# Kernel tuning notes

Measured on AMD Instinct MI355X. Metric: run time of the kernel, lower is better.

## Reference

```python
import jax, jax.numpy as jnp
import numpy as np

B, P, S, H, R = 32, 512, 1024, 1024, 256


def setup_inputs() -> dict:
    key = jax.random.key(0)
    k1, k2, k3 = jax.random.split(key, 3)
    pairs = jax.random.randint(k1, (B, P, 2, 2), 0, S, dtype=jnp.int64 if jax.config.jax_enable_x64 else jnp.int32)
    hidden_states = jax.random.normal(k2, (B, S, H), dtype=jnp.float32)
    W = jax.random.normal(k3, (R, 3 * H), dtype=jnp.float32) * (1.0 / np.sqrt(3 * H))
    b = jnp.zeros((R,), dtype=jnp.float32)
    return {"pairs": pairs, "hidden_states": hidden_states, "W": W, "b": b}


def reference(pairs, hidden_states, W, b):
    # pairs: [B, P, 2, 2] -> [:, :, 0, :] = (h_start, h_end), [:, :, 1, :] = (t_start, t_end)
    def gather_tokens(idx):  # idx: [B, P] -> [B, P, H]
        return jnp.take_along_axis(hidden_states, idx[:, :, None], axis=1)

    head_embed = 0.5 * (gather_tokens(pairs[:, :, 0, 0]) + gather_tokens(pairs[:, :, 0, 1]))
    tail_embed = 0.5 * (gather_tokens(pairs[:, :, 1, 0]) + gather_tokens(pairs[:, :, 1, 1]))
    feats = jnp.concatenate([head_embed, tail_embed, head_embed * tail_embed], axis=-1)  # [B, P, 3H]
    logits = jnp.einsum('bpf,rf->bpr', feats, W) + b  # [B, P, R]
    return logits
```

## Files before the change

kernel.cpp:

```cpp
#include <hip/hip_runtime.h>

#define NB 32
#define NP 512
#define NS 1024
#define NH 1024
#define NR 256
#define K3 3072

#define BM 64

typedef short short8 __attribute__((ext_vector_type(8)));
typedef __bf16 bf16x8 __attribute__((ext_vector_type(8)));
typedef float f32x4 __attribute__((ext_vector_type(4)));

__device__ __forceinline__ unsigned short f2bf(float f) {
  unsigned u = __builtin_bit_cast(unsigned, f);
  u += 0x7fffu + ((u >> 16) & 1u);
  return (unsigned short)(u >> 16);
}

__device__ __forceinline__ f32x4 mfma_bf16(short8 a, short8 b, f32x4 c) {
  return __builtin_amdgcn_mfma_f32_16x16x32_bf16(
      __builtin_bit_cast(bf16x8, a), __builtin_bit_cast(bf16x8, b), c, 0, 0, 0);
}

__device__ __forceinline__ void wg_barrier() {
  asm volatile("s_waitcnt lgkmcnt(0)" ::: "memory");
  __builtin_amdgcn_s_barrier();
}

__global__ void wconv_kernel(const float* __restrict__ W,
                             unsigned short* __restrict__ WbF) {
  int i = blockIdx.x * blockDim.x + threadIdx.x;
  int lane = i & 63, n16 = (i >> 6) & 15, kc = i >> 10;
  int lr = lane & 15, lg = lane >> 4;
  const float* src = W + (size_t)(n16 * 16 + lr) * K3 + kc * 32 + lg * 8;
  float4 a = *(const float4*)src;
  float4 b = *(const float4*)(src + 4);
  short8 o;
  o[0] = (short)f2bf(a.x); o[1] = (short)f2bf(a.y);
  o[2] = (short)f2bf(a.z); o[3] = (short)f2bf(a.w);
  o[4] = (short)f2bf(b.x); o[5] = (short)f2bf(b.y);
  o[6] = (short)f2bf(b.z); o[7] = (short)f2bf(b.w);
  *(short8*)(WbF + (size_t)i * 8) = o;
}

__global__ __launch_bounds__(512, 2) void gemm_kernel(
    const int* __restrict__ pairs, const float* __restrict__ hs,
    const unsigned short* __restrict__ WbF, const float* __restrict__ bias,
    float* __restrict__ out) {
  __shared__ __align__(16) unsigned short sA[2][3][BM][64];

  const int tid = threadIdx.x;
  const int blk = blockIdx.x;
  const int x     = blk & 7;
  const int jb    = blk >> 3;
  const int batch = x * 4 + (jb >> 3);
  const int mtile = jb & 7;
  const int m0    = (batch * 8 + mtile) * BM;

  const int pairi = tid >> 3;
  const int q     = tid & 7;
  int4 pr = ((const int4*)pairs)[m0 + pairi];
  const float* hb = hs + (size_t)batch * NS * NH + 8 * q;
  const float* rp[4];
  rp[0] = hb + (size_t)pr.x * NH;
  rp[1] = hb + (size_t)pr.y * NH;
  rp[2] = hb + (size_t)pr.z * NH;
  rp[3] = hb + (size_t)pr.w * NH;

  const int lane = tid & 63;
  const int w    = tid >> 6;
  const int lr   = lane & 15;
  const int lg   = lane >> 4;

  const unsigned short* wbase = WbF + (size_t)(w * 2) * 512 + (size_t)lane * 8;

  f32x4 acc[4][2];
#pragma unroll
  for (int i = 0; i < 4; ++i)
#pragma unroll
    for (int j = 0; j < 2; ++j) acc[i][j] = (f32x4){0.f, 0.f, 0.f, 0.f};

  float4 ldA[8], ldB[8];
  short8 wcur[12], wnxt[12];

  auto load_w = [&](int s, short8* wd) {
#pragma unroll
    for (int part = 0; part < 3; ++part)
#pragma unroll
      for (int ks = 0; ks < 2; ++ks)
#pragma unroll
        for (int j = 0; j < 2; ++j)
          wd[part * 4 + ks * 2 + j] = *(const short8*)(
              wbase + (size_t)(part * 32 + s * 2 + ks) * 8192 + (size_t)j * 512);
  };

  auto load_gather = [&](int s, float4* ld) {
    const int o = s * 64;
#pragma unroll
    for (int r = 0; r < 4; ++r) {
      ld[2 * r]     = *(const float4*)(rp[r] + o);
      ld[2 * r + 1] = *(const float4*)(rp[r] + o + 4);
    }
  };

  auto store_stage = [&](int buf, const float4* ld) {
    short8 hv, tv, pv;
#pragma unroll
    for (int e = 0; e < 8; ++e) {
      const int hi = e >> 2, ei = e & 3;
      float h = 0.5f * (((const float*)&ld[0 + hi])[ei] + ((const float*)&ld[2 + hi])[ei]);
      float t = 0.5f * (((const float*)&ld[4 + hi])[ei] + ((const float*)&ld[6 + hi])[ei]);
      float p = h * t;
      hv[e] = (short)f2bf(h); tv[e] = (short)f2bf(t); pv[e] = (short)f2bf(p);
    }
    const int col = (q ^ (pairi & 7)) * 8;
    *(short8*)&sA[buf][0][pairi][col] = hv;
    *(short8*)&sA[buf][1][pairi][col] = tv;
    *(short8*)&sA[buf][2][pairi][col] = pv;
  };

  auto compute = [&](int buf, short8* wc) {
#pragma unroll
    for (int ks = 0; ks < 2; ++ks) {
      short8 ah[4], at4[4], ap[4];
      const int col = (((ks * 4 + lg) ^ (lr & 7)) * 8);
#pragma unroll
      for (int i = 0; i < 4; ++i) {
        ah[i]  = *(const short8*)&sA[buf][0][i * 16 + lr][col];
        at4[i] = *(const short8*)&sA[buf][1][i * 16 + lr][col];
        ap[i]  = *(const short8*)&sA[buf][2][i * 16 + lr][col];
      }
#pragma unroll
      for (int j = 0; j < 2; ++j)
#pragma unroll
        for (int i = 0; i < 4; ++i) {
          acc[i][j] = mfma_bf16(ah[i],  wc[0 + ks * 2 + j], acc[i][j]);
          acc[i][j] = mfma_bf16(at4[i], wc[4 + ks * 2 + j], acc[i][j]);
          acc[i][j] = mfma_bf16(ap[i],  wc[8 + ks * 2 + j], acc[i][j]);
        }
    }
  };

  load_w(0, wcur);
  load_gather(0, ldA);
  load_gather(1, ldB);
  store_stage(0, ldA);

  auto stage = [&](int s, short8* wc, short8* wn, float4* gin, float4* gout) {
    wg_barrier();
    if (s < 15) load_w(s + 1, wn);
    if (s < 14) load_gather(s + 2, gin);
    compute(s & 1, wc);
    if (s < 15) store_stage((s & 1) ^ 1, gout);
  };

#pragma unroll 1
  for (int sp = 0; sp < 8; ++sp) {
    stage(2 * sp,     wcur, wnxt, ldA, ldB);
    stage(2 * sp + 1, wnxt, wcur, ldB, ldA);
  }

#pragma unroll
  for (int j = 0; j < 2; ++j) {
    const int col  = w * 32 + j * 16 + lr;
    const float bv = bias[col];
#pragma unroll
    for (int i = 0; i < 4; ++i) {
      const size_t rbase = (size_t)(m0 + i * 16 + lg * 4) * NR + col;
#pragma unroll
      for (int r = 0; r < 4; ++r)
        out[rbase + (size_t)r * NR] = acc[i][j][r] + bv;
    }
  }
}

extern "C" void kernel_launch(void* const* d_in, const int* in_sizes, int n_in,
                              void* d_out, int out_size, void* d_ws, size_t ws_size,
                              hipStream_t stream) {
  const int*   pairs = (const int*)d_in[0];
  const float* hs    = (const float*)d_in[1];
  const float* W     = (const float*)d_in[2];
  const float* bias  = (const float*)d_in[3];
  float* out = (float*)d_out;
  unsigned short* WbF = (unsigned short*)d_ws;

  wconv_kernel<<<(96 * 16 * 64) / 256, 256, 0, stream>>>(W, WbF);
  gemm_kernel<<<(NB * NP) / BM, 512, 0, stream>>>(pairs, hs, WbF, bias, out);
}
```

Before: 230.2 us.

## Pre-convert hidden states to half precision and switch MFMA to fp16

Measured after the change: 244.4 us. 1.06x slower.

```diff
diff --git a/kernel.cpp b/kernel.cpp
--- a/kernel.cpp
+++ b/kernel.cpp
@@ -9,19 +9,11 @@
 
 #define BM 64
 
-typedef short short8 __attribute__((ext_vector_type(8)));
-typedef __bf16 bf16x8 __attribute__((ext_vector_type(8)));
+typedef _Float16 half8 __attribute__((ext_vector_type(8)));
 typedef float f32x4 __attribute__((ext_vector_type(4)));
 
-__device__ __forceinline__ unsigned short f2bf(float f) {
-  unsigned u = __builtin_bit_cast(unsigned, f);
-  u += 0x7fffu + ((u >> 16) & 1u);
-  return (unsigned short)(u >> 16);
-}
-
-__device__ __forceinline__ f32x4 mfma_bf16(short8 a, short8 b, f32x4 c) {
-  return __builtin_amdgcn_mfma_f32_16x16x32_bf16(
-      __builtin_bit_cast(bf16x8, a), __builtin_bit_cast(bf16x8, b), c, 0, 0, 0);
+__device__ __forceinline__ f32x4 mfma_f16(half8 a, half8 b, f32x4 c) {
+  return __builtin_amdgcn_mfma_f32_16x16x32_f16(a, b, c, 0, 0, 0);
 }
 
 __device__ __forceinline__ void wg_barrier() {
@@ -30,26 +22,39 @@
 }
 
 __global__ void wconv_kernel(const float* __restrict__ W,
-                             unsigned short* __restrict__ WbF) {
+                             _Float16* __restrict__ WbF) {
   int i = blockIdx.x * blockDim.x + threadIdx.x;
   int lane = i & 63, n16 = (i >> 6) & 15, kc = i >> 10;
   int lr = lane & 15, lg = lane >> 4;
   const float* src = W + (size_t)(n16 * 16 + lr) * K3 + kc * 32 + lg * 8;
   float4 a = *(const float4*)src;
   float4 b = *(const float4*)(src + 4);
-  short8 o;
-  o[0] = (short)f2bf(a.x); o[1] = (short)f2bf(a.y);
-  o[2] = (short)f2bf(a.z); o[3] = (short)f2bf(a.w);
-  o[4] = (short)f2bf(b.x); o[5] = (short)f2bf(b.y);
-  o[6] = (short)f2bf(b.z); o[7] = (short)f2bf(b.w);
-  *(short8*)(WbF + (size_t)i * 8) = o;
+  half8 o;
+  o[0] = (_Float16)a.x; o[1] = (_Float16)a.y;
+  o[2] = (_Float16)a.z; o[3] = (_Float16)a.w;
+  o[4] = (_Float16)b.x; o[5] = (_Float16)b.y;
+  o[6] = (_Float16)b.z; o[7] = (_Float16)b.w;
+  *(half8*)(WbF + (size_t)i * 8) = o;
+}
+
+__global__ void hconv_kernel(const float* __restrict__ hs,
+                             _Float16* __restrict__ hsH) {
+  size_t i = ((size_t)blockIdx.x * blockDim.x + threadIdx.x) * 8;
+  float4 a = *(const float4*)(hs + i);
+  float4 b = *(const float4*)(hs + i + 4);
+  half8 o;
+  o[0] = (_Float16)(0.5f * a.x); o[1] = (_Float16)(0.5f * a.y);
+  o[2] = (_Float16)(0.5f * a.z); o[3] = (_Float16)(0.5f * a.w);
+  o[4] = (_Float16)(0.5f * b.x); o[5] = (_Float16)(0.5f * b.y);
+  o[6] = (_Float16)(0.5f * b.z); o[7] = (_Float16)(0.5f * b.w);
+  *(half8*)(hsH + i) = o;
 }
 
 __global__ __launch_bounds__(512, 2) void gemm_kernel(
-    const int* __restrict__ pairs, const float* __restrict__ hs,
-    const unsigned short* __restrict__ WbF, const float* __restrict__ bias,
+    const int* __restrict__ pairs, const _Float16* __restrict__ hsH,
+    const _Float16* __restrict__ WbF, const float* __restrict__ bias,
     float* __restrict__ out) {
-  __shared__ __align__(16) unsigned short sA[2][3][BM][64];
+  __shared__ __align__(16) _Float16 sA[2][3][BM][64];
 
   const int tid = threadIdx.x;
   const int blk = blockIdx.x;
@@ -62,8 +67,8 @@
   const int pairi = tid >> 3;
   const int q     = tid & 7;
   int4 pr = ((const int4*)pairs)[m0 + pairi];
-  const float* hb = hs + (size_t)batch * NS * NH + 8 * q;
-  const float* rp[4];
+  const _Float16* hb = hsH + (size_t)batch * NS * NH + 8 * q;
+  const _Float16* rp[4];
   rp[0] = hb + (size_t)pr.x * NH;
   rp[1] = hb + (size_t)pr.y * NH;
   rp[2] = hb + (size_t)pr.z * NH;
@@ -74,7 +79,7 @@
   const int lr   = lane & 15;
   const int lg   = lane >> 4;
 
-  const unsigned short* wbase = WbF + (size_t)(w * 2) * 512 + (size_t)lane * 8;
+  const _Float16* wbase = WbF + (size_t)(w * 2) * 512 + (size_t)lane * 8;
 
   f32x4 acc[4][2];
 #pragma unroll
@@ -82,63 +87,60 @@
 #pragma unroll
     for (int j = 0; j < 2; ++j) acc[i][j] = (f32x4){0.f, 0.f, 0.f, 0.f};
 
-  float4 ldA[8], ldB[8];
-  short8 wcur[12], wnxt[12];
+  half8 ldA[4], ldB[4];
+  half8 wcur[12], wnxt[12];
 
-  auto load_w = [&](int s, short8* wd) {
+  auto load_w = [&](int s, half8* wd) {
 #pragma unroll
     for (int part = 0; part < 3; ++part)
 #pragma unroll
       for (int ks = 0; ks < 2; ++ks)
 #pragma unroll
         for (int j = 0; j < 2; ++j)
-          wd[part * 4 + ks * 2 + j] = *(const short8*)(
+          wd[part * 4 + ks * 2 + j] = *(const half8*)(
               wbase + (size_t)(part * 32 + s * 2 + ks) * 8192 + (size_t)j * 512);
   };
 
-  auto load_gather = [&](int s, float4* ld) {
+  auto load_gather = [&](int s, half8* ld) {
     const int o = s * 64;
 #pragma unroll
-    for (int r = 0; r < 4; ++r) {
-      ld[2 * r]     = *(const float4*)(rp[r] + o);
-      ld[2 * r + 1] = *(const float4*)(rp[r] + o + 4);
-    }
+    for (int r = 0; r < 4; ++r)
+      ld[r] = *(const half8*)(rp[r] + o);
   };
 
-  auto store_stage = [&](int buf, const float4* ld) {
-    short8 hv, tv, pv;
+  auto store_stage = [&](int buf, const half8* ld) {
+    half8 hv, tv, pv;
 #pragma unroll
     for (int e = 0; e < 8; ++e) {
-      const int hi = e >> 2, ei = e & 3;
-      float h = 0.5f * (((const float*)&ld[0 + hi])[ei] + ((const float*)&ld[2 + hi])[ei]);
-      float t = 0.5f * (((const float*)&ld[4 + hi])[ei] + ((const float*)&ld[6 + hi])[ei]);
+      float h = (float)ld[0][e] + (float)ld[1][e];
+      float t = (float)ld[2][e] + (float)ld[3][e];
       float p = h * t;
-      hv[e] = (short)f2bf(h); tv[e] = (short)f2bf(t); pv[e] = (short)f2bf(p);
+      hv[e] = (_Float16)h; tv[e] = (_Float16)t; pv[e] = (_Float16)p;
     }
     const int col = (q ^ (pairi & 7)) * 8;
-    *(short8*)&sA[buf][0][pairi][col] = hv;
-    *(short8*)&sA[buf][1][pairi][col] = tv;
-    *(short8*)&sA[buf][2][pairi][col] = pv;
+    *(half8*)&sA[buf][0][pairi][col] = hv;
+    *(half8*)&sA[buf][1][pairi][col] = tv;
+    *(half8*)&sA[buf][2][pairi][col] = pv;
   };
 
-  auto compute = [&](int buf, short8* wc) {
+  auto compute = [&](int buf, half8* wc) {
 #pragma unroll
     for (int ks = 0; ks < 2; ++ks) {
-      short8 ah[4], at4[4], ap[4];
+      half8 ah[4], at4[4], ap[4];
       const int col = (((ks * 4 + lg) ^ (lr & 7)) * 8);
 #pragma unroll
       for (int i = 0; i < 4; ++i) {
-        ah[i]  = *(const short8*)&sA[buf][0][i * 16 + lr][col];
-        at4[i] = *(const short8*)&sA[buf][1][i * 16 + lr][col];
-        ap[i]  = *(const short8*)&sA[buf][2][i * 16 + lr][col];
+        ah[i]  = *(const half8*)&sA[buf][0][i * 16 + lr][col];
+        at4[i] = *(const half8*)&sA[buf][1][i * 16 + lr][col];
+        ap[i]  = *(const half8*)&sA[buf][2][i * 16 + lr][col];
       }
 #pragma unroll
       for (int j = 0; j < 2; ++j)
 #pragma unroll
         for (int i = 0; i < 4; ++i) {
-          acc[i][j] = mfma_bf16(ah[i],  wc[0 + ks * 2 + j], acc[i][j]);
-          acc[i][j] = mfma_bf16(at4[i], wc[4 + ks * 2 + j], acc[i][j]);
-          acc[i][j] = mfma_bf16(ap[i],  wc[8 + ks * 2 + j], acc[i][j]);
+          acc[i][j] = mfma_f16(ah[i],  wc[0 + ks * 2 + j], acc[i][j]);
+          acc[i][j] = mfma_f16(at4[i], wc[4 + ks * 2 + j], acc[i][j]);
+          acc[i][j] = mfma_f16(ap[i],  wc[8 + ks * 2 + j], acc[i][j]);
         }
     }
   };
@@ -148,7 +150,7 @@
   load_gather(1, ldB);
   store_stage(0, ldA);
 
-  auto stage = [&](int s, short8* wc, short8* wn, float4* gin, float4* gout) {
+  auto stage = [&](int s, half8* wc, half8* wn, half8* gin, half8* gout) {
     wg_barrier();
     if (s < 15) load_w(s + 1, wn);
     if (s < 14) load_gather(s + 2, gin);
@@ -184,8 +186,10 @@
   const float* W     = (const float*)d_in[2];
   const float* bias  = (const float*)d_in[3];
   float* out = (float*)d_out;
-  unsigned short* WbF = (unsigned short*)d_ws;
+  _Float16* WbF = (_Float16*)d_ws;
+  _Float16* hsH = (_Float16*)((char*)d_ws + (2u << 20));
 
   wconv_kernel<<<(96 * 16 * 64) / 256, 256, 0, stream>>>(W, WbF);
-  gemm_kernel<<<(NB * NP) / BM, 512, 0, stream>>>(pairs, hs, WbF, bias, out);
+  hconv_kernel<<<(NB * NS * NH / 8) / 256, 256, 0, stream>>>(hs, hsH);
+  gemm_kernel<<<(NB * NP) / BM, 512, 0, stream>>>(pairs, hsH, WbF, bias, out);
 }
```
